# Performance work log

Hardware: AMD Instinct MI355X
Metric: run time of the kernel (lower is better)

Reference implementation:

```python
import jax, jax.numpy as jnp
import numpy as np

B, D, H, W, C = 2, 28, 28, 28, 96
HEADS = 3
WS = (7, 7, 7)
SS = (3, 3, 3)
N = WS[0] * WS[1] * WS[2]  # 343 tokens per window
MLP_DIM = 4 * C


def _rel_pos_index():
    coords = np.stack(np.meshgrid(np.arange(WS[0]), np.arange(WS[1]), np.arange(WS[2]), indexing='ij'))
    cf = coords.reshape(3, -1)
    rel = (cf[:, :, None] - cf[:, None, :]).transpose(1, 2, 0)
    rel[..., 0] += WS[0] - 1
    rel[..., 1] += WS[1] - 1
    rel[..., 2] += WS[2] - 1
    rel[..., 0] *= (2 * WS[1] - 1) * (2 * WS[2] - 1)
    rel[..., 1] *= 2 * WS[2] - 1
    return rel.sum(-1)  # [N, N] int


def _compute_mask():
    # shifted-window attention mask (MONAI compute_mask)
    img = np.zeros((1, D, H, W, 1), np.float32)
    cnt = 0.0
    for ds in (slice(0, -WS[0]), slice(-WS[0], -SS[0]), slice(-SS[0], None)):
        for hs in (slice(0, -WS[1]), slice(-WS[1], -SS[1]), slice(-SS[1], None)):
            for ws_ in (slice(0, -WS[2]), slice(-WS[2], -SS[2]), slice(-SS[2], None)):
                img[:, ds, hs, ws_, :] = cnt
                cnt += 1.0
    mw = img.reshape(1, D // WS[0], WS[0], H // WS[1], WS[1], W // WS[2], WS[2], 1)
    mw = mw.transpose(0, 1, 3, 5, 2, 4, 6, 7).reshape(-1, N)  # [nw, N]
    diff = mw[:, None, :] - mw[:, :, None]
    return np.where(diff != 0, -100.0, 0.0).astype(np.float32)  # [nw, N, N]


def _ln(x, g, b):
    mu = x.mean(-1, keepdims=True)
    var = ((x - mu) ** 2).mean(-1, keepdims=True)
    return (x - mu) * jax.lax.rsqrt(var + 1e-5) * g + b


def setup_inputs() -> dict:
    key = jax.random.key(0)
    ks = jax.random.split(key, 8)
    f = lambda k, shape: (jax.random.normal(k, shape) * 0.02).astype(jnp.float32)
    n_bias = (2 * WS[0] - 1) * (2 * WS[1] - 1) * (2 * WS[2] - 1)
    return {
        'x': jax.random.normal(ks[0], (B, D, H, W, C), jnp.float32),
        'mask_matrix': jnp.asarray(_compute_mask()),
        'g1': jnp.ones((C,), jnp.float32), 'b1': jnp.zeros((C,), jnp.float32),
        'w_qkv': f(ks[1], (3 * C, C)), 'b_qkv': jnp.zeros((3 * C,), jnp.float32),
        'bias_table': f(ks[2], (n_bias, HEADS)),
        'w_proj': f(ks[3], (C, C)), 'b_proj': jnp.zeros((C,), jnp.float32),
        'g2': jnp.ones((C,), jnp.float32), 'b2': jnp.zeros((C,), jnp.float32),
        'w_fc1': f(ks[4], (MLP_DIM, C)), 'b_fc1': jnp.zeros((MLP_DIM,), jnp.float32),
        'w_fc2': f(ks[5], (C, MLP_DIM)), 'b_fc2': jnp.zeros((C,), jnp.float32),
        'rel_index': jnp.asarray(_rel_pos_index(), dtype=jnp.int32),
    }


def reference(x, mask_matrix, g1, b1, w_qkv, b_qkv, bias_table, w_proj, b_proj,
              g2, b2, w_fc1, b_fc1, w_fc2, b_fc2, rel_index):
    shortcut = x
    h = _ln(x, g1, b1)
    # cyclic shift
    h = jnp.roll(h, (-SS[0], -SS[1], -SS[2]), axis=(1, 2, 3))
    # window partition -> [B_, N, C]
    win = h.reshape(B, D // WS[0], WS[0], H // WS[1], WS[1], W // WS[2], WS[2], C)
    win = win.transpose(0, 1, 3, 5, 2, 4, 6, 7).reshape(-1, N, C)
    Bw = win.shape[0]
    hd = C // HEADS
    qkv = (win @ w_qkv.T + b_qkv).reshape(Bw, N, 3, HEADS, hd).transpose(2, 0, 3, 1, 4)
    q, k, v = qkv[0] * (hd ** -0.5), qkv[1], qkv[2]
    attn = jnp.einsum('bhnd,bhmd->bhnm', q, k)  # [Bw, H, N, N]
    bias = bias_table[rel_index.reshape(-1)].reshape(N, N, HEADS).transpose(2, 0, 1)
    attn = attn + bias[None]
    nw = mask_matrix.shape[0]
    attn = attn.reshape(Bw // nw, nw, HEADS, N, N) + mask_matrix[None, :, None]
    attn = jax.nn.softmax(attn.reshape(Bw, HEADS, N, N), axis=-1)
    out = jnp.einsum('bhnm,bhmd->bhnd', attn, v).transpose(0, 2, 1, 3).reshape(Bw, N, C)
    out = out @ w_proj.T + b_proj
    # window reverse -> [B, D, H, W, C]
    out = out.reshape(B, D // WS[0], H // WS[1], W // WS[2], WS[0], WS[1], WS[2], C)
    out = out.transpose(0, 1, 4, 2, 5, 3, 6, 7).reshape(B, D, H, W, C)
    # reverse cyclic shift
    out = jnp.roll(out, SS, axis=(1, 2, 3))
    x = shortcut + out
    h2 = _ln(x, g2, b2)
    h2 = jax.nn.gelu(h2 @ w_fc1.T + b_fc1, approximate=False)
    return x + (h2 @ w_fc2.T + b_fc2)
```

## Files before the change

kernel.cpp:

```cpp
#include <hip/hip_runtime.h>
#include <hip/hip_bf16.h>

typedef unsigned short u16;
typedef unsigned int u32;
typedef unsigned char u8;

#define T_TOK 43904
#define NTOK 343

typedef __attribute__((ext_vector_type(4))) float f32x4;
typedef __attribute__((ext_vector_type(8))) short s16x8;

__device__ __forceinline__ float bf2f(u32 v) { return __uint_as_float(v << 16); }
__device__ __forceinline__ u16 f2bf(float f) {
  u32 u = __float_as_uint(f);
  return (u16)((u + 0x7fffu + ((u >> 16) & 1u)) >> 16);
}

__device__ __forceinline__ float ldf(const void* p, int f32, size_t i) {
  return f32 ? ((const float*)p)[i] : bf2f(((const u16*)p)[i]);
}
__device__ __forceinline__ float2 ld2(const void* p, int f32, size_t i) {
  if (f32) return *(const float2*)((const float*)p + i);
  u32 pk = *(const u32*)((const u16*)p + i);
  return make_float2(bf2f(pk & 0xffff), bf2f(pk >> 16));
}

__device__ __forceinline__ size_t spatial_base(int t) {
  int win = t / 343, n = t - win * 343;
  int bb = win >> 6, wrem = win & 63;
  int wd = wrem >> 4, wh = (wrem >> 2) & 3, ww = wrem & 3;
  int td = n / 49; int r = n - td * 49; int th = r / 7; int tw = r - th * 7;
  int d0 = wd * 7 + td + 3; if (d0 >= 28) d0 -= 28;
  int h0 = wh * 7 + th + 3; if (h0 >= 28) h0 -= 28;
  int w0 = ww * 7 + tw + 3; if (w0 >= 28) w0 -= 28;
  return (size_t)(((bb * 28 + d0) * 28 + h0) * 28 + w0) * 96;
}

__device__ __forceinline__ int zone3(int p) { return p < 21 ? 0 : (p < 25 ? 1 : 2); }
__device__ __forceinline__ int cid_of(int mw, int n) {
  int td = n / 49, rr = n - td * 49, th = rr / 7, tw = rr - th * 7;
  int d = (mw >> 4) * 7 + td, h = ((mw >> 2) & 3) * 7 + th, w = (mw & 3) * 7 + tw;
  return zone3(d) * 9 + zone3(h) * 3 + zone3(w);
}

__global__ __launch_bounds__(64) void detect_kernel(const u16* __restrict__ x, int* __restrict__ flag) {
  int lane = threadIdx.x;
  int bad = 0;
  #pragma unroll
  for (int q = 0; q < 8; q++) {
    u16 b = x[(lane * 8 + q) * 2];
    int e = (b >> 7) & 0xff;
    if (e >= 0x90) bad = 1;
  }
  unsigned long long m = __ballot(bad);
  if (lane == 0) *flag = (m != 0ull) ? 1 : 0;
}

__global__ __launch_bounds__(256) void wconv_kernel(
    const void* __restrict__ w0, const void* __restrict__ w1,
    const void* __restrict__ w2, const void* __restrict__ w3,
    u16* __restrict__ out, const int* __restrict__ dflag) {
  int f32 = __builtin_amdgcn_readfirstlane(dflag[0]);
  int g = blockIdx.x * 256 + threadIdx.x;
  if (g >= 110592) return;
  float v;
  if (g < 27648)      v = ldf(w0, f32, g);
  else if (g < 36864) v = ldf(w1, f32, g - 27648);
  else if (g < 73728) v = ldf(w2, f32, g - 36864);
  else                v = ldf(w3, f32, g - 73728);
  out[g] = f2bf(v);
}

__global__ __launch_bounds__(256) void ln_gather_kernel(
    const void* __restrict__ x, const void* __restrict__ g, const void* __restrict__ b,
    u16* __restrict__ outw, const int* __restrict__ dflag) {
  int f32 = __builtin_amdgcn_readfirstlane(dflag[0]);
  int t = blockIdx.x * 4 + (threadIdx.x >> 6);
  int lane = threadIdx.x & 63;
  size_t base = spatial_base(t);
  int c = lane * 2;
  float vx = 0.f, vy = 0.f;
  if (c < 96) { float2 p = ld2(x, f32, base + c); vx = p.x; vy = p.y; }
  float s = vx + vy, ss = vx * vx + vy * vy;
  #pragma unroll
  for (int o = 1; o < 64; o <<= 1) { s += __shfl_xor(s, o); ss += __shfl_xor(ss, o); }
  float mean = s * (1.f / 96.f);
  float var = ss * (1.f / 96.f) - mean * mean;
  float rstd = rsqrtf(var + 1e-5f);
  if (c < 96) {
    float2 gp = ld2(g, f32, c), bp = ld2(b, f32, c);
    float y0 = (vx - mean) * rstd * gp.x + bp.x;
    float y1 = (vy - mean) * rstd * gp.y + bp.y;
    *(u32*)(outw + (size_t)t * 96 + c) = (u32)f2bf(y0) | ((u32)f2bf(y1) << 16);
  }
}

__global__ __launch_bounds__(256) void b3_kernel(
    const void* __restrict__ bias_table, const int* __restrict__ rel,
    u16* __restrict__ b3, const int* __restrict__ dflag) {
  int f32 = __builtin_amdgcn_readfirstlane(dflag[0]);
  int row = blockIdx.x, head = blockIdx.y;
  for (int c = threadIdx.x; c < 352; c += 256) {
    u16 v = 0;
    if (c < 343) v = f2bf(ldf(bias_table, f32, (size_t)rel[row * 343 + c] * 3 + head));
    b3[((size_t)head * 343 + row) * 352 + c] = v;
  }
}

template <int MODE>
__global__ __launch_bounds__(256) void gemm_mfma_kernel(
    const u16* __restrict__ A, const u16* __restrict__ Wb, const void* __restrict__ bias,
    const void* __restrict__ xg, const u16* __restrict__ xres_in,
    const void* __restrict__ gg, const void* __restrict__ bb,
    u16* __restrict__ out2, void* __restrict__ outp,
    int K, int N, const int* __restrict__ dflag) {
  int f32 = __builtin_amdgcn_readfirstlane(dflag[0]);
  __shared__ alignas(16) u16 As[128 * 104];
  __shared__ alignas(16) u16 Ws[96 * 104];
  int tid = threadIdx.x;
  int m0 = blockIdx.x * 128, n0 = blockIdx.y * 96;
  int w = tid >> 6, lane = tid & 63, quad = lane >> 4, l16 = lane & 15;
  f32x4 acc[2][6];
  #pragma unroll
  for (int i = 0; i < 2; i++)
    #pragma unroll
    for (int j = 0; j < 6; j++) acc[i][j] = (f32x4){0.f, 0.f, 0.f, 0.f};

  for (int kb = 0; kb < K; kb += 96) {
    if (kb) __syncthreads();
    for (int i = tid; i < 1536; i += 256) {
      int row = i / 12; int c = (i - row * 12) * 8;
      *(uint4*)&As[row * 104 + c] = *(const uint4*)(A + (size_t)(m0 + row) * K + kb + c);
    }
    for (int i = tid; i < 1152; i += 256) {
      int row = i / 12; int c = (i - row * 12) * 8;
      *(uint4*)&Ws[row * 104 + c] = *(const uint4*)(Wb + (size_t)(n0 + row) * K + kb + c);
    }
    __syncthreads();
    #pragma unroll
    for (int kc = 0; kc < 3; kc++) {
      s16x8 fa0 = *(const s16x8*)&As[(w * 32 + l16) * 104 + kc * 32 + quad * 8];
      s16x8 fa1 = *(const s16x8*)&As[(w * 32 + 16 + l16) * 104 + kc * 32 + quad * 8];
      #pragma unroll
      for (int j = 0; j < 6; j++) {
        s16x8 fb = *(const s16x8*)&Ws[(j * 16 + l16) * 104 + kc * 32 + quad * 8];
        acc[0][j] = __builtin_amdgcn_mfma_f32_16x16x32_bf16(fa0, fb, acc[0][j], 0, 0, 0);
        acc[1][j] = __builtin_amdgcn_mfma_f32_16x16x32_bf16(fa1, fb, acc[1][j], 0, 0, 0);
      }
    }
  }
  float bv[6], gv[6], b2v[6];
  #pragma unroll
  for (int j = 0; j < 6; j++) {
    int nn = n0 + j * 16 + l16;
    bv[j] = ldf(bias, f32, nn);
    if (MODE == 2) { gv[j] = ldf(gg, f32, nn); b2v[j] = ldf(bb, f32, nn); }
  }
  #pragma unroll
  for (int i = 0; i < 2; i++) {
    #pragma unroll
    for (int r = 0; r < 4; r++) {
      int mm = m0 + w * 32 + i * 16 + quad * 4 + r;
      size_t sb = (MODE == 2 || MODE == 3) ? spatial_base(mm) : 0;
      if (MODE == 2) {
        float rv[6];
        float s = 0.f, ss = 0.f;
        #pragma unroll
        for (int j = 0; j < 6; j++) {
          int nn = j * 16 + l16;
          float v = acc[i][j][r] + bv[j] + ldf(xg, f32, sb + nn);
          rv[j] = v; s += v; ss += v * v;
          ((u16*)outp)[(size_t)mm * 96 + nn] = f2bf(v);
        }
        #pragma unroll
        for (int o = 1; o < 16; o <<= 1) { s += __shfl_xor(s, o); ss += __shfl_xor(ss, o); }
        float mean = s * (1.f / 96.f);
        float var = ss * (1.f / 96.f) - mean * mean;
        float rstd = rsqrtf(var + 1e-5f);
        #pragma unroll
        for (int j = 0; j < 6; j++) {
          int nn = j * 16 + l16;
          out2[(size_t)mm * 96 + nn] = f2bf((rv[j] - mean) * rstd * gv[j] + b2v[j]);
        }
      } else {
        #pragma unroll
        for (int j = 0; j < 6; j++) {
          int nn = n0 + j * 16 + l16;
          float v = acc[i][j][r] + bv[j];
          if (MODE == 1) {
            v = 0.5f * v * (1.0f + erff(v * 0.70710678118f));
            ((u16*)outp)[(size_t)mm * N + nn] = f2bf(v);
          } else if (MODE == 3) {
            float rr = bf2f(xres_in[(size_t)mm * 96 + nn]) + v;
            if (f32) ((float*)outp)[sb + nn] = rr;
            else     ((u16*)outp)[sb + nn] = f2bf(rr);
          } else {
            int sel = nn / 96, hd = (nn - sel * 96) >> 5, cc = nn & 31;
            float scl = (sel == 0) ? 0.17677669529663687f : 1.0f;
            ((u16*)outp)[((size_t)(sel * 3 + hd) * T_TOK + mm) * 32 + cc] = f2bf(v * scl);
          }
        }
      }
    }
  }
}

__global__ __launch_bounds__(256) void attn_mfma_kernel(
    const u16* __restrict__ qkv, const u16* __restrict__ b3,
    u16* __restrict__ attnb) {
  __shared__ alignas(16) u16 Ks[344 * 32];
  __shared__ alignas(16) u8  cidk[352];
  __shared__ alignas(16) u16 Vt[32 * 352];
  __shared__ alignas(16) u16 Ps[4][512];

  int tid = threadIdx.x;
  int wh = blockIdx.y;
  int head = wh % 3;
  int win = wh / 3;
  int mw = win & 63;
  int m0 = blockIdx.x * 64;
  size_t wbase = (size_t)win * NTOK;

  const u16* qplane = qkv + ((size_t)head * T_TOK + wbase) * 32;
  const u16* kplane = qkv + ((size_t)(3 + head) * T_TOK + wbase) * 32;
  const u16* vplane = qkv + ((size_t)(6 + head) * T_TOK + wbase) * 32;

  for (int i = tid; i < 1376; i += 256) {
    int tok = i >> 2, cb = i & 3;
    uint4 kv = make_uint4(0, 0, 0, 0);
    if (tok < 343) kv = *(const uint4*)(kplane + (size_t)tok * 32 + cb * 8);
    *(uint4*)&Ks[tok * 32 + 8 * (cb ^ (tok & 3))] = kv;
  }
  for (int i = tid; i < 688; i += 256) {
    int p = i >> 2, cb = (i & 3) * 8;
    int t0 = 2 * p;
    uint4 v0 = *(const uint4*)(vplane + (size_t)t0 * 32 + cb);
    uint4 v1 = make_uint4(0, 0, 0, 0);
    if (t0 + 1 < 343) v1 = *(const uint4*)(vplane + (size_t)(t0 + 1) * 32 + cb);
    u32 a0[4] = {v0.x, v0.y, v0.z, v0.w};
    u32 a1[4] = {v1.x, v1.y, v1.z, v1.w};
    int blk = t0 >> 3, tin = (t0 & 7) >> 1;
    #pragma unroll
    for (int q = 0; q < 4; q++) {
      int ch0 = cb + 2 * q;
      u32 w0v = (a0[q] & 0xffffu) | ((a1[q] & 0xffffu) << 16);
      u32 w1v = (a0[q] >> 16) | (a1[q] & 0xffff0000u);
      ((u32*)Vt)[ch0 * 176 + 4 * (blk ^ ((ch0 >> 1) & 3)) + tin] = w0v;
      ((u32*)Vt)[(ch0 + 1) * 176 + 4 * (blk ^ ((ch0 >> 1) & 3)) + tin] = w1v;
    }
  }
  {
    int ch = tid >> 3, j = tid & 7;
    if (tid < 256) Vt[ch * 352 + 8 * (43 ^ ((ch >> 1) & 3)) + j] = 0;
  }
  for (int n = tid; n < 352; n += 256) cidk[n] = (n < 343) ? (u8)cid_of(mw, n) : (u8)255;
  __syncthreads();

  int w = tid >> 6, lane = tid & 63, quad = lane >> 4, l16 = lane & 15;
  int qbase = m0 + w * 16;
  int qrow_l = qbase + l16;
  int qc = qrow_l < NTOK ? qrow_l : NTOK - 1;
  s16x8 fq = *(const s16x8*)(qplane + (size_t)qrow_l * 32 + quad * 8);
  int cq = cid_of(mw, qc);
  const u16* b3row = b3 + ((size_t)head * 343 + qc) * 352;

  float lsum = 0.f;
  f32x4 o0 = {0.f, 0.f, 0.f, 0.f}, o1 = {0.f, 0.f, 0.f, 0.f};
  const f32x4 zz = {0.f, 0.f, 0.f, 0.f};
  int swl = l16 & 3;
  int vsw0 = (l16 >> 1) & 3, vsw1 = ((16 + l16) >> 1) & 3;

  for (int t32 = 0; t32 < 11; t32++) {
    #pragma unroll
    for (int h = 0; h < 2; h++) {
      int kb = t32 * 32 + h * 16;
      int ktok = kb + l16;
      s16x8 fk = *(const s16x8*)&Ks[ktok * 32 + 8 * (quad ^ (ktok & 3))];
      f32x4 st = __builtin_amdgcn_mfma_f32_16x16x32_bf16(fk, fq, zz, 0, 0, 0);
      #pragma unroll
      for (int r = 0; r < 4; r++) {
        int key = kb + quad * 4 + r;
        float sv = st[r] + bf2f(b3row[key]) + ((cq == (int)cidk[key]) ? 0.f : -100.f);
        float p = __expf(sv);
        lsum += p;
        int k32 = h * 16 + quad * 4 + r;
        Ps[w][l16 * 32 + 8 * ((k32 >> 3) ^ swl) + (k32 & 7)] = f2bf(p);
      }
    }
    s16x8 fp  = *(const s16x8*)&Ps[w][l16 * 32 + 8 * (quad ^ swl)];
    s16x8 fv0 = *(const s16x8*)&Vt[l16 * 352 + 8 * ((t32 * 4 + quad) ^ vsw0)];
    s16x8 fv1 = *(const s16x8*)&Vt[(16 + l16) * 352 + 8 * ((t32 * 4 + quad) ^ vsw1)];
    o0 = __builtin_amdgcn_mfma_f32_16x16x32_bf16(fp, fv0, o0, 0, 0, 0);
    o1 = __builtin_amdgcn_mfma_f32_16x16x32_bf16(fp, fv1, o1, 0, 0, 0);
  }

  lsum += __shfl_xor(lsum, 16);
  lsum += __shfl_xor(lsum, 32);
  #pragma unroll
  for (int r = 0; r < 4; r++) {
    int qrow = qbase + quad * 4 + r;
    float ls = __shfl(lsum, quad * 4 + r);
    if (qrow < NTOK) {
      float rs = 1.0f / ls;
      size_t ob = (wbase + qrow) * 96 + head * 32;
      attnb[ob + l16] = f2bf(o0[r] * rs);
      attnb[ob + 16 + l16] = f2bf(o1[r] * rs);
    }
  }
}

extern "C" void kernel_launch(void* const* d_in, const int* in_sizes, int n_in,
                              void* d_out, int out_size, void* d_ws, size_t ws_size,
                              hipStream_t stream) {
  (void)in_sizes; (void)n_in; (void)out_size; (void)ws_size;
  const void* x       = d_in[0];
  const void* g1      = d_in[2];
  const void* b1      = d_in[3];
  const void* w_qkv   = d_in[4];
  const void* b_qkv   = d_in[5];
  const void* bias_tb = d_in[6];
  const void* w_proj  = d_in[7];
  const void* b_proj  = d_in[8];
  const void* g2      = d_in[9];
  const void* b2      = d_in[10];
  const void* w_fc1   = d_in[11];
  const void* b_fc1   = d_in[12];
  const void* w_fc2   = d_in[13];
  const void* b_fc2   = d_in[14];
  const int* rel_idx  = (const int*)d_in[15];

  char* ws = (char*)d_ws;
  int*  dflag = (int*)ws;
  u16*  winb  = (u16*)(ws + 256);
  u16*  xresb = (u16*)(ws + 256 + 8429568);
  u16*  qkvb  = (u16*)(ws + 256 + 2 * 8429568);
  u16*  attnb = (u16*)(ws + 256 + 2 * 8429568 + 25288704);
  u16*  h2b   = (u16*)(ws + 256 + 2 * 8429568);
  u16*  b3b   = (u16*)(ws + 256 + 2 * 8429568 + 33718272);
  u16*  wcat  = (u16*)(ws + 256 + 2 * 8429568 + 33718272 + 724416);
  u16*  w_qkvb = wcat;
  u16*  w_projb = wcat + 27648;
  u16*  w_fc1b = wcat + 36864;
  u16*  w_fc2b = wcat + 73728;

  detect_kernel<<<1, 64, 0, stream>>>((const u16*)x, dflag);
  wconv_kernel<<<432, 256, 0, stream>>>(w_qkv, w_proj, w_fc1, w_fc2, wcat, dflag);
  b3_kernel<<<dim3(343, 3), 256, 0, stream>>>(bias_tb, rel_idx, b3b, dflag);
  ln_gather_kernel<<<T_TOK / 4, 256, 0, stream>>>(x, g1, b1, winb, dflag);
  gemm_mfma_kernel<4><<<dim3(343, 3), 256, 0, stream>>>(
      winb, w_qkvb, b_qkv, nullptr, nullptr, nullptr, nullptr, nullptr, qkvb, 96, 288, dflag);
  attn_mfma_kernel<<<dim3(6, 384), 256, 0, stream>>>(qkvb, b3b, attnb);
  gemm_mfma_kernel<2><<<dim3(343, 1), 256, 0, stream>>>(
      attnb, w_projb, b_proj, x, nullptr, g2, b2, winb, xresb, 96, 96, dflag);
  gemm_mfma_kernel<1><<<dim3(343, 4), 256, 0, stream>>>(
      winb, w_fc1b, b_fc1, nullptr, nullptr, nullptr, nullptr, nullptr, h2b, 96, 384, dflag);
  gemm_mfma_kernel<3><<<dim3(343, 1), 256, 0, stream>>>(
      h2b, w_fc2b, b_fc2, nullptr, xresb, nullptr, nullptr, nullptr, d_out, 384, 96, dflag);
}
```

Measured before the change: 258.5 us.

## Fuse proj/LN/MLP into one kernel, precombine bias+mask, exp2 softmax

Replaces the three post-attention GEMM launches with one fused kernel that does proj, residual, LayerNorm2, fc1+GELU and fc2 per 64-row tile in LDS. This removes the xres and h2 round trips to global memory. The attention mask is folded into a per-class bias table pre-scaled by log2e, so the attention loop uses exp2 and drops the cid compare. Attention now runs 512-thread blocks, stores P with packed, truncated bf16 writes, and uses a changed V swizzle. The fused MLP kernel has fewer blocks and reloads weights per chunk, which may lower occupancy and parallelism.

```diff
diff --git a/kernel.cpp b/kernel.cpp
--- a/kernel.cpp
+++ b/kernel.cpp
@@ -1,5 +1,6 @@
 #include <hip/hip_runtime.h>
 #include <hip/hip_bf16.h>
+#include <math.h>
 
 typedef unsigned short u16;
 typedef unsigned int u32;
@@ -7,6 +8,8 @@
 
 #define T_TOK 43904
 #define NTOK 343
+#define LOG2E 1.4426950408889634f
+#define MASKV 144.26950408889634f
 
 typedef __attribute__((ext_vector_type(4))) float f32x4;
 typedef __attribute__((ext_vector_type(8))) short s16x8;
@@ -96,25 +99,28 @@
   }
 }
 
-__global__ __launch_bounds__(256) void b3_kernel(
+__global__ __launch_bounds__(256) void b3m_kernel(
     const void* __restrict__ bias_table, const int* __restrict__ rel,
-    u16* __restrict__ b3, const int* __restrict__ dflag) {
+    u16* __restrict__ b3m, const int* __restrict__ dflag) {
   int f32 = __builtin_amdgcn_readfirstlane(dflag[0]);
-  int row = blockIdx.x, head = blockIdx.y;
-  for (int c = threadIdx.x; c < 352; c += 256) {
-    u16 v = 0;
-    if (c < 343) v = f2bf(ldf(bias_table, f32, (size_t)rel[row * 343 + c] * 3 + head));
-    b3[((size_t)head * 343 + row) * 352 + c] = v;
-  }
-}
-
-template <int MODE>
-__global__ __launch_bounds__(256) void gemm_mfma_kernel(
+  int row = blockIdx.x;
+  int by = blockIdx.y;
+  int cls = by / 3, head = by - cls * 3;
+  int mw = ((cls & 4) ? 48 : 0) | ((cls & 2) ? 12 : 0) | ((cls & 1) ? 3 : 0);
+  int cidq = cid_of(mw, row);
+  for (int col = threadIdx.x; col < 352; col += 256) {
+    float v = -MASKV;
+    if (col < 343) {
+      v = ldf(bias_table, f32, (size_t)rel[row * 343 + col] * 3 + head) * LOG2E;
+      if (cid_of(mw, col) != cidq) v -= MASKV;
+    }
+    b3m[((size_t)by * 343 + row) * 352 + col] = f2bf(v);
+  }
+}
+
+__global__ __launch_bounds__(256) void qkv_kernel(
     const u16* __restrict__ A, const u16* __restrict__ Wb, const void* __restrict__ bias,
-    const void* __restrict__ xg, const u16* __restrict__ xres_in,
-    const void* __restrict__ gg, const void* __restrict__ bb,
-    u16* __restrict__ out2, void* __restrict__ outp,
-    int K, int N, const int* __restrict__ dflag) {
+    u16* __restrict__ outp, const int* __restrict__ dflag) {
   int f32 = __builtin_amdgcn_readfirstlane(dflag[0]);
   __shared__ alignas(16) u16 As[128 * 104];
   __shared__ alignas(16) u16 Ws[96 * 104];
@@ -126,113 +132,72 @@
   for (int i = 0; i < 2; i++)
     #pragma unroll
     for (int j = 0; j < 6; j++) acc[i][j] = (f32x4){0.f, 0.f, 0.f, 0.f};
-
-  for (int kb = 0; kb < K; kb += 96) {
-    if (kb) __syncthreads();
-    for (int i = tid; i < 1536; i += 256) {
-      int row = i / 12; int c = (i - row * 12) * 8;
-      *(uint4*)&As[row * 104 + c] = *(const uint4*)(A + (size_t)(m0 + row) * K + kb + c);
-    }
-    for (int i = tid; i < 1152; i += 256) {
-      int row = i / 12; int c = (i - row * 12) * 8;
-      *(uint4*)&Ws[row * 104 + c] = *(const uint4*)(Wb + (size_t)(n0 + row) * K + kb + c);
-    }
-    __syncthreads();
-    #pragma unroll
-    for (int kc = 0; kc < 3; kc++) {
-      s16x8 fa0 = *(const s16x8*)&As[(w * 32 + l16) * 104 + kc * 32 + quad * 8];
-      s16x8 fa1 = *(const s16x8*)&As[(w * 32 + 16 + l16) * 104 + kc * 32 + quad * 8];
+  for (int i = tid; i < 1536; i += 256) {
+    int row = i / 12; int c = (i - row * 12) * 8;
+    *(uint4*)&As[row * 104 + c] = *(const uint4*)(A + (size_t)(m0 + row) * 96 + c);
+  }
+  for (int i = tid; i < 1152; i += 256) {
+    int row = i / 12; int c = (i - row * 12) * 8;
+    *(uint4*)&Ws[row * 104 + c] = *(const uint4*)(Wb + (size_t)(n0 + row) * 96 + c);
+  }
+  __syncthreads();
+  #pragma unroll
+  for (int kc = 0; kc < 3; kc++) {
+    s16x8 fa0 = *(const s16x8*)&As[(w * 32 + l16) * 104 + kc * 32 + quad * 8];
+    s16x8 fa1 = *(const s16x8*)&As[(w * 32 + 16 + l16) * 104 + kc * 32 + quad * 8];
+    #pragma unroll
+    for (int j = 0; j < 6; j++) {
+      s16x8 fb = *(const s16x8*)&Ws[(j * 16 + l16) * 104 + kc * 32 + quad * 8];
+      acc[0][j] = __builtin_amdgcn_mfma_f32_16x16x32_bf16(fa0, fb, acc[0][j], 0, 0, 0);
+      acc[1][j] = __builtin_amdgcn_mfma_f32_16x16x32_bf16(fa1, fb, acc[1][j], 0, 0, 0);
+    }
+  }
+  #pragma unroll
+  for (int i = 0; i < 2; i++) {
+    #pragma unroll
+    for (int r = 0; r < 4; r++) {
+      int mm = m0 + w * 32 + i * 16 + quad * 4 + r;
       #pragma unroll
       for (int j = 0; j < 6; j++) {
-        s16x8 fb = *(const s16x8*)&Ws[(j * 16 + l16) * 104 + kc * 32 + quad * 8];
-        acc[0][j] = __builtin_amdgcn_mfma_f32_16x16x32_bf16(fa0, fb, acc[0][j], 0, 0, 0);
-        acc[1][j] = __builtin_amdgcn_mfma_f32_16x16x32_bf16(fa1, fb, acc[1][j], 0, 0, 0);
+        int nn = n0 + j * 16 + l16;
+        float v = acc[i][j][r] + ldf(bias, f32, nn);
+        int sel = nn / 96, hd = (nn - sel * 96) >> 5, cc = nn & 31;
+        float scl = (sel == 0) ? 0.25504208f : 1.0f;
+        outp[((size_t)(sel * 3 + hd) * T_TOK + mm) * 32 + cc] = f2bf(v * scl);
       }
     }
   }
-  float bv[6], gv[6], b2v[6];
-  #pragma unroll
-  for (int j = 0; j < 6; j++) {
-    int nn = n0 + j * 16 + l16;
-    bv[j] = ldf(bias, f32, nn);
-    if (MODE == 2) { gv[j] = ldf(gg, f32, nn); b2v[j] = ldf(bb, f32, nn); }
-  }
-  #pragma unroll
-  for (int i = 0; i < 2; i++) {
-    #pragma unroll
-    for (int r = 0; r < 4; r++) {
-      int mm = m0 + w * 32 + i * 16 + quad * 4 + r;
-      size_t sb = (MODE == 2 || MODE == 3) ? spatial_base(mm) : 0;
-      if (MODE == 2) {
-        float rv[6];
-        float s = 0.f, ss = 0.f;
-        #pragma unroll
-        for (int j = 0; j < 6; j++) {
-          int nn = j * 16 + l16;
-          float v = acc[i][j][r] + bv[j] + ldf(xg, f32, sb + nn);
-          rv[j] = v; s += v; ss += v * v;
-          ((u16*)outp)[(size_t)mm * 96 + nn] = f2bf(v);
-        }
-        #pragma unroll
-        for (int o = 1; o < 16; o <<= 1) { s += __shfl_xor(s, o); ss += __shfl_xor(ss, o); }
-        float mean = s * (1.f / 96.f);
-        float var = ss * (1.f / 96.f) - mean * mean;
-        float rstd = rsqrtf(var + 1e-5f);
-        #pragma unroll
-        for (int j = 0; j < 6; j++) {
-          int nn = j * 16 + l16;
-          out2[(size_t)mm * 96 + nn] = f2bf((rv[j] - mean) * rstd * gv[j] + b2v[j]);
-        }
-      } else {
-        #pragma unroll
-        for (int j = 0; j < 6; j++) {
-          int nn = n0 + j * 16 + l16;
-          float v = acc[i][j][r] + bv[j];
-          if (MODE == 1) {
-            v = 0.5f * v * (1.0f + erff(v * 0.70710678118f));
-            ((u16*)outp)[(size_t)mm * N + nn] = f2bf(v);
-          } else if (MODE == 3) {
-            float rr = bf2f(xres_in[(size_t)mm * 96 + nn]) + v;
-            if (f32) ((float*)outp)[sb + nn] = rr;
-            else     ((u16*)outp)[sb + nn] = f2bf(rr);
-          } else {
-            int sel = nn / 96, hd = (nn - sel * 96) >> 5, cc = nn & 31;
-            float scl = (sel == 0) ? 0.17677669529663687f : 1.0f;
-            ((u16*)outp)[((size_t)(sel * 3 + hd) * T_TOK + mm) * 32 + cc] = f2bf(v * scl);
-          }
-        }
-      }
-    }
-  }
-}
-
-__global__ __launch_bounds__(256) void attn_mfma_kernel(
-    const u16* __restrict__ qkv, const u16* __restrict__ b3,
+}
+
+__device__ __forceinline__ int vsw(int ch) { return ((ch >> 1) ^ (ch >> 3)) & 3; }
+
+__global__ __launch_bounds__(512) void attn_mfma_kernel(
+    const u16* __restrict__ qkv, const u16* __restrict__ b3m,
     u16* __restrict__ attnb) {
-  __shared__ alignas(16) u16 Ks[344 * 32];
-  __shared__ alignas(16) u8  cidk[352];
+  __shared__ alignas(16) u16 Ks[352 * 32];
   __shared__ alignas(16) u16 Vt[32 * 352];
-  __shared__ alignas(16) u16 Ps[4][512];
+  __shared__ alignas(16) u16 Ps[8][512];
 
   int tid = threadIdx.x;
   int wh = blockIdx.y;
   int head = wh % 3;
   int win = wh / 3;
   int mw = win & 63;
-  int m0 = blockIdx.x * 64;
+  int cls = (((mw >> 4) == 3) ? 4 : 0) | ((((mw >> 2) & 3) == 3) ? 2 : 0) | (((mw & 3) == 3) ? 1 : 0);
+  int m0 = blockIdx.x * 128;
   size_t wbase = (size_t)win * NTOK;
 
   const u16* qplane = qkv + ((size_t)head * T_TOK + wbase) * 32;
   const u16* kplane = qkv + ((size_t)(3 + head) * T_TOK + wbase) * 32;
   const u16* vplane = qkv + ((size_t)(6 + head) * T_TOK + wbase) * 32;
 
-  for (int i = tid; i < 1376; i += 256) {
+  for (int i = tid; i < 1408; i += 512) {
     int tok = i >> 2, cb = i & 3;
     uint4 kv = make_uint4(0, 0, 0, 0);
     if (tok < 343) kv = *(const uint4*)(kplane + (size_t)tok * 32 + cb * 8);
     *(uint4*)&Ks[tok * 32 + 8 * (cb ^ (tok & 3))] = kv;
   }
-  for (int i = tid; i < 688; i += 256) {
+  for (int i = tid; i < 688; i += 512) {
     int p = i >> 2, cb = (i & 3) * 8;
     int t0 = 2 * p;
     uint4 v0 = *(const uint4*)(vplane + (size_t)t0 * 32 + cb);
@@ -246,30 +211,28 @@
       int ch0 = cb + 2 * q;
       u32 w0v = (a0[q] & 0xffffu) | ((a1[q] & 0xffffu) << 16);
       u32 w1v = (a0[q] >> 16) | (a1[q] & 0xffff0000u);
-      ((u32*)Vt)[ch0 * 176 + 4 * (blk ^ ((ch0 >> 1) & 3)) + tin] = w0v;
-      ((u32*)Vt)[(ch0 + 1) * 176 + 4 * (blk ^ ((ch0 >> 1) & 3)) + tin] = w1v;
-    }
-  }
-  {
+      ((u32*)Vt)[ch0 * 176 + 4 * (blk ^ vsw(ch0)) + tin] = w0v;
+      ((u32*)Vt)[(ch0 + 1) * 176 + 4 * (blk ^ vsw(ch0 + 1)) + tin] = w1v;
+    }
+  }
+  if (tid < 256) {
     int ch = tid >> 3, j = tid & 7;
-    if (tid < 256) Vt[ch * 352 + 8 * (43 ^ ((ch >> 1) & 3)) + j] = 0;
-  }
-  for (int n = tid; n < 352; n += 256) cidk[n] = (n < 343) ? (u8)cid_of(mw, n) : (u8)255;
+    Vt[ch * 352 + 8 * (43 ^ vsw(ch)) + j] = 0;
+  }
   __syncthreads();
 
   int w = tid >> 6, lane = tid & 63, quad = lane >> 4, l16 = lane & 15;
   int qbase = m0 + w * 16;
   int qrow_l = qbase + l16;
   int qc = qrow_l < NTOK ? qrow_l : NTOK - 1;
-  s16x8 fq = *(const s16x8*)(qplane + (size_t)qrow_l * 32 + quad * 8);
-  int cq = cid_of(mw, qc);
-  const u16* b3row = b3 + ((size_t)head * 343 + qc) * 352;
+  s16x8 fq = *(const s16x8*)(qplane + (size_t)qc * 32 + quad * 8);
+  const u16* bmrow = b3m + ((size_t)(cls * 3 + head) * 343 + qc) * 352;
+  int swl = (l16 ^ (l16 >> 2)) & 3;
+  int vsw0 = vsw(l16), vsw1 = vsw(16 + l16);
 
   float lsum = 0.f;
   f32x4 o0 = {0.f, 0.f, 0.f, 0.f}, o1 = {0.f, 0.f, 0.f, 0.f};
   const f32x4 zz = {0.f, 0.f, 0.f, 0.f};
-  int swl = l16 & 3;
-  int vsw0 = (l16 >> 1) & 3, vsw1 = ((16 + l16) >> 1) & 3;
 
   for (int t32 = 0; t32 < 11; t32++) {
     #pragma unroll
@@ -278,15 +241,16 @@
       int ktok = kb + l16;
       s16x8 fk = *(const s16x8*)&Ks[ktok * 32 + 8 * (quad ^ (ktok & 3))];
       f32x4 st = __builtin_amdgcn_mfma_f32_16x16x32_bf16(fk, fq, zz, 0, 0, 0);
-      #pragma unroll
-      for (int r = 0; r < 4; r++) {
-        int key = kb + quad * 4 + r;
-        float sv = st[r] + bf2f(b3row[key]) + ((cq == (int)cidk[key]) ? 0.f : -100.f);
-        float p = __expf(sv);
-        lsum += p;
-        int k32 = h * 16 + quad * 4 + r;
-        Ps[w][l16 * 32 + 8 * ((k32 >> 3) ^ swl) + (k32 & 7)] = f2bf(p);
-      }
+      uint2 bm = *(const uint2*)(bmrow + kb + quad * 4);
+      float p0 = exp2f(st[0] + bf2f(bm.x & 0xffff));
+      float p1 = exp2f(st[1] + bf2f(bm.x >> 16));
+      float p2 = exp2f(st[2] + bf2f(bm.y & 0xffff));
+      float p3 = exp2f(st[3] + bf2f(bm.y >> 16));
+      lsum += (p0 + p1) + (p2 + p3);
+      u32 pa = (__float_as_uint(p0) >> 16) | (__float_as_uint(p1) & 0xffff0000u);
+      u32 pb = (__float_as_uint(p2) >> 16) | (__float_as_uint(p3) & 0xffff0000u);
+      int blkp = h * 2 + (quad >> 1);
+      *(uint2*)&Ps[w][l16 * 32 + 8 * (blkp ^ swl) + (quad & 1) * 4] = make_uint2(pa, pb);
     }
     s16x8 fp  = *(const s16x8*)&Ps[w][l16 * 32 + 8 * (quad ^ swl)];
     s16x8 fv0 = *(const s16x8*)&Vt[l16 * 352 + 8 * ((t32 * 4 + quad) ^ vsw0)];
@@ -306,6 +270,135 @@
       size_t ob = (wbase + qrow) * 96 + head * 32;
       attnb[ob + l16] = f2bf(o0[r] * rs);
       attnb[ob + 16 + l16] = f2bf(o1[r] * rs);
+    }
+  }
+}
+
+__global__ __launch_bounds__(256) void mlp_fused_kernel(
+    const u16* __restrict__ attnb, const u16* __restrict__ wcat,
+    const void* __restrict__ x, const void* __restrict__ b_proj,
+    const void* __restrict__ g2, const void* __restrict__ b2,
+    const void* __restrict__ b_fc1, const void* __restrict__ b_fc2,
+    void* __restrict__ outp, const int* __restrict__ dflag) {
+  int f32 = __builtin_amdgcn_readfirstlane(dflag[0]);
+  __shared__ alignas(16) u16 As[64 * 104];
+  __shared__ alignas(16) u16 As2[64 * 104];
+  __shared__ alignas(16) u16 Ws[96 * 104];
+  const u16* w_projb = wcat + 27648;
+  const u16* w_fc1b  = wcat + 36864;
+  const u16* w_fc2b  = wcat + 73728;
+  int tid = threadIdx.x, m0 = blockIdx.x * 64;
+  int w = tid >> 6, lane = tid & 63, quad = lane >> 4, l16 = lane & 15;
+
+  for (int i = tid; i < 768; i += 256) {
+    int row = i / 12, c = (i - row * 12) * 8;
+    *(uint4*)&As[row * 104 + c] = *(const uint4*)(attnb + (size_t)(m0 + row) * 96 + c);
+  }
+  for (int i = tid; i < 1152; i += 256) {
+    int row = i / 12, c = (i - row * 12) * 8;
+    *(uint4*)&Ws[row * 104 + c] = *(const uint4*)(w_projb + row * 96 + c);
+  }
+  __syncthreads();
+  f32x4 accp[6];
+  #pragma unroll
+  for (int j = 0; j < 6; j++) accp[j] = (f32x4){0.f, 0.f, 0.f, 0.f};
+  #pragma unroll
+  for (int kc = 0; kc < 3; kc++) {
+    s16x8 fa = *(const s16x8*)&As[(w * 16 + l16) * 104 + kc * 32 + quad * 8];
+    #pragma unroll
+    for (int j = 0; j < 6; j++) {
+      s16x8 fb = *(const s16x8*)&Ws[(j * 16 + l16) * 104 + kc * 32 + quad * 8];
+      accp[j] = __builtin_amdgcn_mfma_f32_16x16x32_bf16(fa, fb, accp[j], 0, 0, 0);
+    }
+  }
+  __syncthreads();
+
+  float bp[6], gv[6], b2v[6];
+  #pragma unroll
+  for (int j = 0; j < 6; j++) {
+    int nn = j * 16 + l16;
+    bp[j] = ldf(b_proj, f32, nn); gv[j] = ldf(g2, f32, nn); b2v[j] = ldf(b2, f32, nn);
+  }
+  float rv[4][6];
+  size_t sb[4];
+  #pragma unroll
+  for (int r = 0; r < 4; r++) {
+    int mm = m0 + w * 16 + quad * 4 + r;
+    sb[r] = spatial_base(mm);
+    float s = 0.f, ss = 0.f;
+    #pragma unroll
+    for (int j = 0; j < 6; j++) {
+      float v = accp[j][r] + bp[j] + ldf(x, f32, sb[r] + j * 16 + l16);
+      rv[r][j] = v; s += v; ss += v * v;
+    }
+    #pragma unroll
+    for (int o = 1; o < 16; o <<= 1) { s += __shfl_xor(s, o); ss += __shfl_xor(ss, o); }
+    float mean = s * (1.f / 96.f);
+    float var = ss * (1.f / 96.f) - mean * mean;
+    float rstd = rsqrtf(var + 1e-5f);
+    #pragma unroll
+    for (int j = 0; j < 6; j++)
+      As[(w * 16 + quad * 4 + r) * 104 + j * 16 + l16] = f2bf((rv[r][j] - mean) * rstd * gv[j] + b2v[j]);
+  }
+
+  f32x4 acc2[6];
+  #pragma unroll
+  for (int j = 0; j < 6; j++) acc2[j] = (f32x4){0.f, 0.f, 0.f, 0.f};
+  for (int c = 0; c < 4; c++) {
+    __syncthreads();
+    for (int i = tid; i < 1152; i += 256) {
+      int row = i / 12, cc = (i - row * 12) * 8;
+      *(uint4*)&Ws[row * 104 + cc] = *(const uint4*)(w_fc1b + (size_t)(96 * c + row) * 96 + cc);
+    }
+    __syncthreads();
+    f32x4 a1[6];
+    #pragma unroll
+    for (int j = 0; j < 6; j++) a1[j] = (f32x4){0.f, 0.f, 0.f, 0.f};
+    #pragma unroll
+    for (int kc = 0; kc < 3; kc++) {
+      s16x8 fa = *(const s16x8*)&As[(w * 16 + l16) * 104 + kc * 32 + quad * 8];
+      #pragma unroll
+      for (int j = 0; j < 6; j++) {
+        s16x8 fb = *(const s16x8*)&Ws[(j * 16 + l16) * 104 + kc * 32 + quad * 8];
+        a1[j] = __builtin_amdgcn_mfma_f32_16x16x32_bf16(fa, fb, a1[j], 0, 0, 0);
+      }
+    }
+    #pragma unroll
+    for (int j = 0; j < 6; j++) {
+      float bf1 = ldf(b_fc1, f32, 96 * c + j * 16 + l16);
+      #pragma unroll
+      for (int r = 0; r < 4; r++) {
+        float v = a1[j][r] + bf1;
+        v = 0.5f * v * (1.0f + erff(v * 0.70710678118f));
+        As2[(w * 16 + quad * 4 + r) * 104 + j * 16 + l16] = f2bf(v);
+      }
+    }
+    __syncthreads();
+    for (int i = tid; i < 1152; i += 256) {
+      int row = i / 12, cc = (i - row * 12) * 8;
+      *(uint4*)&Ws[row * 104 + cc] = *(const uint4*)(w_fc2b + (size_t)row * 384 + 96 * c + cc);
+    }
+    __syncthreads();
+    #pragma unroll
+    for (int kc = 0; kc < 3; kc++) {
+      s16x8 fa2 = *(const s16x8*)&As2[(w * 16 + l16) * 104 + kc * 32 + quad * 8];
+      #pragma unroll
+      for (int j = 0; j < 6; j++) {
+        s16x8 fb = *(const s16x8*)&Ws[(j * 16 + l16) * 104 + kc * 32 + quad * 8];
+        acc2[j] = __builtin_amdgcn_mfma_f32_16x16x32_bf16(fa2, fb, acc2[j], 0, 0, 0);
+      }
+    }
+  }
+  float bf2v[6];
+  #pragma unroll
+  for (int j = 0; j < 6; j++) bf2v[j] = ldf(b_fc2, f32, j * 16 + l16);
+  #pragma unroll
+  for (int r = 0; r < 4; r++) {
+    #pragma unroll
+    for (int j = 0; j < 6; j++) {
+      float v = acc2[j][r] + bf2v[j] + rv[r][j];
+      if (f32) ((float*)outp)[sb[r] + j * 16 + l16] = v;
+      else     ((u16*)outp)[sb[r] + j * 16 + l16] = f2bf(v);
     }
   }
 }
@@ -333,28 +426,18 @@
   char* ws = (char*)d_ws;
   int*  dflag = (int*)ws;
   u16*  winb  = (u16*)(ws + 256);
-  u16*  xresb = (u16*)(ws + 256 + 8429568);
-  u16*  qkvb  = (u16*)(ws + 256 + 2 * 8429568);
-  u16*  attnb = (u16*)(ws + 256 + 2 * 8429568 + 25288704);
-  u16*  h2b   = (u16*)(ws + 256 + 2 * 8429568);
-  u16*  b3b   = (u16*)(ws + 256 + 2 * 8429568 + 33718272);
-  u16*  wcat  = (u16*)(ws + 256 + 2 * 8429568 + 33718272 + 724416);
+  u16*  qkvb  = (u16*)(ws + 8429824);
+  u16*  attnb = (u16*)(ws + 33718528);
+  u16*  b3mb  = (u16*)(ws + 42148096);
+  u16*  wcat  = (u16*)(ws + 47943424);
   u16*  w_qkvb = wcat;
-  u16*  w_projb = wcat + 27648;
-  u16*  w_fc1b = wcat + 36864;
-  u16*  w_fc2b = wcat + 73728;
 
   detect_kernel<<<1, 64, 0, stream>>>((const u16*)x, dflag);
   wconv_kernel<<<432, 256, 0, stream>>>(w_qkv, w_proj, w_fc1, w_fc2, wcat, dflag);
-  b3_kernel<<<dim3(343, 3), 256, 0, stream>>>(bias_tb, rel_idx, b3b, dflag);
+  b3m_kernel<<<dim3(343, 24), 256, 0, stream>>>(bias_tb, rel_idx, b3mb, dflag);
   ln_gather_kernel<<<T_TOK / 4, 256, 0, stream>>>(x, g1, b1, winb, dflag);
-  gemm_mfma_kernel<4><<<dim3(343, 3), 256, 0, stream>>>(
-      winb, w_qkvb, b_qkv, nullptr, nullptr, nullptr, nullptr, nullptr, qkvb, 96, 288, dflag);
-  attn_mfma_kernel<<<dim3(6, 384), 256, 0, stream>>>(qkvb, b3b, attnb);
-  gemm_mfma_kernel<2><<<dim3(343, 1), 256, 0, stream>>>(
-      attnb, w_projb, b_proj, x, nullptr, g2, b2, winb, xresb, 96, 96, dflag);
-  gemm_mfma_kernel<1><<<dim3(343, 4), 256, 0, stream>>>(
-      winb, w_fc1b, b_fc1, nullptr, nullptr, nullptr, nullptr, nullptr, h2b, 96, 384, dflag);
-  gemm_mfma_kernel<3><<<dim3(343, 1), 256, 0, stream>>>(
-      h2b, w_fc2b, b_fc2, nullptr, xresb, nullptr, nullptr, nullptr, d_out, 384, 96, dflag);
-}
+  qkv_kernel<<<dim3(343, 3), 256, 0, stream>>>(winb, w_qkvb, b_qkv, qkvb, dflag);
+  attn_mfma_kernel<<<dim3(3, 384), 512, 0, stream>>>(qkvb, b3mb, attnb);
+  mlp_fused_kernel<<<686, 256, 0, stream>>>(attnb, wcat, x, b_proj, g2, b2,
+                                            b_fc1, b_fc2, d_out, dflag);
+}
```

After: 228.7 us. 1.13x faster.
